# Kernel optimization log

Measured on AMD Instinct MI355X. Metric: run time of the kernel, lower is better.

Reference implementation:

```python
import jax, jax.numpy as jnp
import numpy as np

HIDDEN = 2048
NUM_HEADS = 16
HEAD_DIM = 128
WINDOW = 1024
ROPE_THETA = 10000.0
B, L = 1, 4096


def setup_inputs() -> dict:
    key = jax.random.key(0)
    k0, k1, k2, k3, k4 = jax.random.split(key, 5)
    s = 1.0 / np.sqrt(HIDDEN)
    return {
        "hidden_states": jax.random.normal(k0, (B, L, HIDDEN), dtype=jnp.float32),
        "wq": jax.random.normal(k1, (HIDDEN, NUM_HEADS * HEAD_DIM), dtype=jnp.float32) * s,
        "wk": jax.random.normal(k2, (HIDDEN, NUM_HEADS * HEAD_DIM), dtype=jnp.float32) * s,
        "wv": jax.random.normal(k3, (HIDDEN, NUM_HEADS * HEAD_DIM), dtype=jnp.float32) * s,
        "wo": jax.random.normal(k4, (NUM_HEADS * HEAD_DIM, HIDDEN), dtype=jnp.float32) * s,
    }


def _apply_rotary(x, cos, sin):
    # x: [B, H, L, D]; cos/sin: [L, D/2]
    d2 = x.shape[-1] // 2
    x1, x2 = x[..., :d2], x[..., d2:]
    return jnp.concatenate([x1 * cos - x2 * sin, x2 * cos + x1 * sin], axis=-1)


def reference(hidden_states, wq, wk, wv, wo):
    Bsz, Ln, _ = hidden_states.shape
    dtype = hidden_states.dtype
    scale = HEAD_DIM ** (-0.5)

    def split_heads(x):
        return x.reshape(Bsz, Ln, NUM_HEADS, HEAD_DIM).transpose(0, 2, 1, 3)

    q = split_heads(hidden_states @ wq)
    k = split_heads(hidden_states @ wk)
    v = split_heads(hidden_states @ wv)

    inv_freq = 1.0 / (ROPE_THETA ** (jnp.arange(0, HEAD_DIM, 2, dtype=jnp.float32) / HEAD_DIM))
    pos = jnp.arange(Ln, dtype=jnp.float32)
    freqs = pos[:, None] * inv_freq[None, :]  # [L, D/2]
    cos = jnp.cos(freqs).astype(dtype)
    sin = jnp.sin(freqs).astype(dtype)

    q = _apply_rotary(q, cos, sin)
    k = _apply_rotary(k, cos, sin)

    q_pos = jnp.arange(Ln)[:, None]
    k_pos = jnp.arange(Ln)[None, :]
    valid = (k_pos > q_pos - WINDOW) & (k_pos <= q_pos)  # [L, L]
    neg = jnp.finfo(dtype).min

    attn = jnp.einsum("bhqd,bhkd->bhqk", q, k) * scale
    attn = jnp.where(valid, attn, neg)
    attn = jax.nn.softmax(attn, axis=-1)
    out = jnp.einsum("bhqk,bhkd->bhqd", attn, v)
    out = out.transpose(0, 2, 1, 3).reshape(Bsz, Ln, NUM_HEADS * HEAD_DIM)
    return out @ wo
```

## Files before the change

kernel.cpp:

```cpp
#include <hip/hip_runtime.h>
#include <cstdint>
#include <cstddef>

typedef unsigned short u16;
typedef __bf16 bf16x8 __attribute__((ext_vector_type(8)));
typedef float f32x4 __attribute__((ext_vector_type(4)));
typedef unsigned short u16x8 __attribute__((ext_vector_type(8)));

#define SEQ 4096
#define HID 2048
#define NH 16
#define HD 128
#define WIN 1024

__device__ __forceinline__ float bf2f(u16 u) {
  union { unsigned int i; float f; } v; v.i = ((unsigned int)u) << 16; return v.f;
}
__device__ __forceinline__ u16 f2bf(float f) {
  union { float f; unsigned int i; } v; v.f = f;
  unsigned int r = v.i + 0x7FFFu + ((v.i >> 16) & 1u);
  return (u16)(r >> 16);
}
__device__ __forceinline__ u16 f2bf_rne(float f) {
  union { __bf16 b; u16 u; } v; v.b = (__bf16)f; return v.u;
}
__device__ __forceinline__ float exp2a(float x) {
  float r; asm("v_exp_f32 %0, %1" : "=v"(r) : "v"(x)); return r;
}
template<int L2R>
__device__ __forceinline__ unsigned swz(unsigned o) { return o ^ (((o >> L2R) & 7u) << 4); }

__device__ __forceinline__ void gload_lds16(const u16* g, u16* l) {
  __builtin_amdgcn_global_load_lds((const __attribute__((address_space(1))) void*)g,
                                   (__attribute__((address_space(3))) void*)l, 16, 0, 0);
}


__global__ void cast_f32_bf16(const float* __restrict__ in, u16* __restrict__ out, int n4) {
  int i = blockIdx.x * blockDim.x + threadIdx.x;
  if (i < n4) {
    float4 v = ((const float4*)in)[i];
    union { u16 u[4]; unsigned long long ll; } r;
    r.u[0] = f2bf(v.x); r.u[1] = f2bf(v.y); r.u[2] = f2bf(v.z); r.u[3] = f2bf(v.w);
    ((unsigned long long*)out)[i] = r.ll;
  }
}

__global__ void transpose_cast4(const float* __restrict__ w0, const float* __restrict__ w1,
                                const float* __restrict__ w2, const float* __restrict__ w3,
                                u16* __restrict__ o0, u16* __restrict__ o1,
                                u16* __restrict__ o2, u16* __restrict__ o3) {
  __shared__ float t[32][33];
  const float* W = (blockIdx.z == 0) ? w0 : (blockIdx.z == 1) ? w1 : (blockIdx.z == 2) ? w2 : w3;
  u16* Wt = (blockIdx.z == 0) ? o0 : (blockIdx.z == 1) ? o1 : (blockIdx.z == 2) ? o2 : o3;
  const int tx = threadIdx.x & 31, ty = threadIdx.x >> 5;
  const int x0 = blockIdx.x * 32, y0 = blockIdx.y * 32;
#pragma unroll
  for (int i = 0; i < 4; ++i)
    t[ty + i * 8][tx] = W[(size_t)(y0 + ty + i * 8) * HID + x0 + tx];
  __syncthreads();
#pragma unroll
  for (int i = 0; i < 4; ++i)
    Wt[(size_t)(x0 + ty + i * 8) * HID + y0 + tx] = f2bf(t[tx][ty + i * 8]);
}

__global__ void rope_table(float* __restrict__ ctab, float* __restrict__ stab) {
  int idx = blockIdx.x * blockDim.x + threadIdx.x;
  int pos = idx >> 6, i = idx & 63;
  float invf = expf(-(float)i * 0.14391156831212787f);
  float ang = (float)pos * invf;
  float s, c;
  sincosf(ang, &s, &c);
  ctab[idx] = c; stab[idx] = s;
}


__global__ __launch_bounds__(256, 2) void gemm_qkv_kernel(
    const u16* __restrict__ X, const u16* __restrict__ Wqt, const u16* __restrict__ Wkt,
    const u16* __restrict__ Wvt, u16* __restrict__ Qo, u16* __restrict__ Ko, u16* __restrict__ Vo,
    const float* __restrict__ ctab, const float* __restrict__ stab) {
  __shared__ u16 ldsA[2][8192];
  __shared__ u16 ldsB[2][8192];
  int flat = (blockIdx.z * 32 + blockIdx.y) * 16 + blockIdx.x;
  int nf = (flat & 7) * 192 + (flat >> 3);
  int bx = nf & 15, by = (nf >> 4) & 31, bz = nf >> 9;
  const u16* Bt = (bz == 0) ? Wqt : (bz == 1) ? Wkt : Wvt;
  u16* Cp = (bz == 0) ? Qo : (bz == 1) ? Ko : Vo;
  const int brow = by * 128, bcol = bx * 128;

  const int lane = threadIdx.x & 63;
  const int wv = threadIdx.x >> 6;
  const int g = lane >> 4, c = lane & 15;
  const int K = HID, N = HID;

  const f32x4 zero = {0.f, 0.f, 0.f, 0.f};
  f32x4 acc[2][8];
#pragma unroll
  for (int m = 0; m < 2; ++m)
#pragma unroll
    for (int n = 0; n < 8; ++n) acc[m][n] = zero;

  auto stage = [&](int buf, int kt) {
    const int k0 = kt * 64;
#pragma unroll
    for (int i = 0; i < 4; ++i) {
      unsigned o = ((unsigned)(wv * 4 + i) * 64 + (unsigned)lane) * 16u;
      unsigned r = o >> 7;
      unsigned cb = swz<7>(o) & 127u;
      const size_t gcol = (size_t)k0 + (cb >> 1);
      gload_lds16(X + (size_t)(brow + r) * K + gcol, &ldsA[buf][(wv * 4 + i) * 512]);
      gload_lds16(Bt + (size_t)(bcol + r) * K + gcol, &ldsB[buf][(wv * 4 + i) * 512]);
    }
  };

  stage(0, 0);
  __syncthreads();
  int buf = 0;
  const int nt = K / 64;
  for (int kt = 0; kt < nt; ++kt) {
    if (kt + 1 < nt) stage(buf ^ 1, kt + 1);
    __builtin_amdgcn_s_setprio(1);
#pragma unroll
    for (int s = 0; s < 2; ++s) {
      const unsigned kb = (unsigned)(s * 64 + g * 16);
      bf16x8 af[2], bfv[8];
#pragma unroll
      for (int m = 0; m < 2; ++m) {
        unsigned row = wv * 32 + m * 16 + c;
        af[m] = *(const bf16x8*)((const char*)&ldsA[buf][0] + swz<7>(row * 128 + kb));
      }
#pragma unroll
      for (int n = 0; n < 8; ++n) {
        unsigned row = n * 16 + c;
        bfv[n] = *(const bf16x8*)((const char*)&ldsB[buf][0] + swz<7>(row * 128 + kb));
      }
#pragma unroll
      for (int m = 0; m < 2; ++m)
#pragma unroll
        for (int n = 0; n < 8; ++n)
          acc[m][n] = __builtin_amdgcn_mfma_f32_16x16x32_bf16(af[m], bfv[n], acc[m][n], 0, 0, 0);
    }
    __builtin_amdgcn_s_setprio(0);
    __syncthreads();
    buf ^= 1;
  }

  if (bz < 2) {
#pragma unroll
    for (int m = 0; m < 2; ++m) {
      const int rbase = brow + wv * 32 + m * 16 + g * 4;
#pragma unroll
      for (int r = 0; r < 4; ++r) {
        const int pos = rbase + r;
        const float* cp = ctab + (size_t)pos * 64;
        const float* sp = stab + (size_t)pos * 64;
        u16* crow = Cp + (size_t)pos * N + bcol;
#pragma unroll
        for (int n = 0; n < 4; ++n) {
          const int i = n * 16 + c;
          const float x1 = acc[m][n][r], x2 = acc[m][n + 4][r];
          const float co = cp[i], si = sp[i];
          crow[i] = f2bf(x1 * co - x2 * si);
          crow[i + 64] = f2bf(x2 * co + x1 * si);
        }
      }
    }
  } else {
#pragma unroll
    for (int m = 0; m < 2; ++m) {
      const int rbase = brow + wv * 32 + m * 16 + g * 4;
#pragma unroll
      for (int r = 0; r < 4; ++r) {
        u16* crow = Cp + (size_t)(rbase + r) * N + bcol;
#pragma unroll
        for (int n = 0; n < 8; ++n)
          crow[n * 16 + c] = f2bf(acc[m][n][r]);
      }
    }
  }
}


__global__ __launch_bounds__(256, 2) void gemm_out_kernel(
    const u16* __restrict__ Ob, const u16* __restrict__ Wot, float* __restrict__ out) {
  __shared__ u16 ldsA[2][8192];
  __shared__ u16 ldsB[2][8192];
  int flat = blockIdx.y * 16 + blockIdx.x;
  int nf = (flat & 7) * 64 + (flat >> 3);
  int bx = nf & 15, by = nf >> 4;
  const int brow = by * 128, bcol = bx * 128;

  const int lane = threadIdx.x & 63;
  const int wv = threadIdx.x >> 6;
  const int wr = wv >> 1, wc = wv & 1;
  const int g = lane >> 4, c = lane & 15;
  const int K = HID, N = HID;

  const f32x4 zero = {0.f, 0.f, 0.f, 0.f};
  f32x4 acc[4][4];
#pragma unroll
  for (int m = 0; m < 4; ++m)
#pragma unroll
    for (int n = 0; n < 4; ++n) acc[m][n] = zero;

  auto stage = [&](int buf, int kt) {
    const int k0 = kt * 64;
#pragma unroll
    for (int i = 0; i < 4; ++i) {
      unsigned o = ((unsigned)(wv * 4 + i) * 64 + (unsigned)lane) * 16u;
      unsigned r = o >> 7;
      unsigned cb = swz<7>(o) & 127u;
      const size_t gcol = (size_t)k0 + (cb >> 1);
      gload_lds16(Ob + (size_t)(brow + r) * K + gcol, &ldsA[buf][(wv * 4 + i) * 512]);
      gload_lds16(Wot + (size_t)(bcol + r) * K + gcol, &ldsB[buf][(wv * 4 + i) * 512]);
    }
  };

  stage(0, 0);
  __syncthreads();
  int buf = 0;
  const int nt = K / 64;
  for (int kt = 0; kt < nt; ++kt) {
    if (kt + 1 < nt) stage(buf ^ 1, kt + 1);
    __builtin_amdgcn_s_setprio(1);
#pragma unroll
    for (int s = 0; s < 2; ++s) {
      const unsigned kb = (unsigned)(s * 64 + g * 16);
      bf16x8 af[4], bfv[4];
#pragma unroll
      for (int m = 0; m < 4; ++m) {
        unsigned row = wr * 64 + m * 16 + c;
        af[m] = *(const bf16x8*)((const char*)&ldsA[buf][0] + swz<7>(row * 128 + kb));
      }
#pragma unroll
      for (int n = 0; n < 4; ++n) {
        unsigned row = wc * 64 + n * 16 + c;
        bfv[n] = *(const bf16x8*)((const char*)&ldsB[buf][0] + swz<7>(row * 128 + kb));
      }
#pragma unroll
      for (int m = 0; m < 4; ++m)
#pragma unroll
        for (int n = 0; n < 4; ++n)
          acc[m][n] = __builtin_amdgcn_mfma_f32_16x16x32_bf16(af[m], bfv[n], acc[m][n], 0, 0, 0);
    }
    __builtin_amdgcn_s_setprio(0);
    __syncthreads();
    buf ^= 1;
  }

#pragma unroll
  for (int m = 0; m < 4; ++m) {
    const int rbase = brow + wr * 64 + m * 16 + g * 4;
#pragma unroll
    for (int n = 0; n < 4; ++n) {
      const int cbase = bcol + wc * 64 + n * 16 + c;
#pragma unroll
      for (int r = 0; r < 4; ++r)
        out[(size_t)(rbase + r) * N + cbase] = acc[m][n][r];
    }
  }
}


__global__ __launch_bounds__(256, 2) void attn_kernel(
    const u16* __restrict__ Q, const u16* __restrict__ K,
    const u16* __restrict__ V, u16* __restrict__ O) {
  __shared__ u16 k_lds[2][8192];
  __shared__ u16 vt_lds[2][8192];
  __shared__ u16 p_lds[4][1024];

  const int lane = threadIdx.x & 63;
  const int wv = threadIdx.x >> 6;
  const int g = lane >> 4;
  const int c = lane & 15;

  int flat = blockIdx.y * 64 + blockIdx.x;
  int nf = (flat & 7) * 128 + (flat >> 3);
  const int q0 = (nf & 63) * 64;
  const int h = nf >> 6;

#pragma unroll
  for (int i = 0; i < 4; ++i) {
    unsigned o = ((unsigned)(wv * 4 + i) * 64 + (unsigned)lane) * 16u;
    unsigned r = o >> 8;
    unsigned cb = swz<8>(o) & 255u;
    gload_lds16(Q + (size_t)(q0 + r) * HID + h * HD + (cb >> 1), &k_lds[0][(wv * 4 + i) * 512]);
  }
  __syncthreads();
  bf16x8 qf[4];
#pragma unroll
  for (int s = 0; s < 4; ++s) {
    unsigned row = wv * 16 + c;
    qf[s] = *(const bf16x8*)((const char*)&k_lds[0][0] + swz<8>(row * 256 + s * 64 + g * 16));
  }
  __syncthreads();

  const int t_start = (q0 >= WIN) ? (q0 - WIN) : 0;

#pragma unroll
  for (int i = 0; i < 4; ++i) {
    unsigned o = ((unsigned)(wv * 4 + i) * 64 + (unsigned)lane) * 16u;
    unsigned r = o >> 8;
    unsigned cb = swz<8>(o) & 255u;
    gload_lds16(K + (size_t)(t_start + r) * HID + h * HD + (cb >> 1), &k_lds[0][(wv * 4 + i) * 512]);
  }
  {
    const u16x8* src = (const u16x8*)(V + (size_t)(t_start + lane) * HID + h * HD + wv * 32);
#pragma unroll
    for (int it = 0; it < 4; ++it) {
      u16x8 vv = src[it];
#pragma unroll
      for (int j = 0; j < 8; ++j) {
        const int d = wv * 32 + it * 8 + j;
        vt_lds[0][d * 64 + (lane ^ ((d & 7) << 3))] = vv[j];
      }
    }
  }
  __syncthreads();

  const f32x4 zero = {0.f, 0.f, 0.f, 0.f};
  float mrow[4], lrow[4];
  f32x4 oacc[8];
#pragma unroll
  for (int r = 0; r < 4; ++r) { mrow[r] = -1e30f; lrow[r] = 0.f; }
#pragma unroll
  for (int d = 0; d < 8; ++d) oacc[d] = zero;

  const float scale2 = 0.12751743f;
  int b = 0;

  for (int t0 = t_start; t0 <= q0; t0 += 64) {
    const int nb = b ^ 1;
    const bool has_next = (t0 + 64 <= q0);

    u16x8 vr[4];
    if (has_next) {
#pragma unroll
      for (int i = 0; i < 4; ++i) {
        unsigned o = ((unsigned)(wv * 4 + i) * 64 + (unsigned)lane) * 16u;
        unsigned r = o >> 8;
        unsigned cb = swz<8>(o) & 255u;
        gload_lds16(K + (size_t)(t0 + 64 + r) * HID + h * HD + (cb >> 1),
                    &k_lds[nb][(wv * 4 + i) * 512]);
      }
      const u16x8* src = (const u16x8*)(V + (size_t)(t0 + 64 + lane) * HID + h * HD + wv * 32);
#pragma unroll
      for (int it = 0; it < 4; ++it) vr[it] = src[it];
    }

    f32x4 sa[4];
#pragma unroll
    for (int kf = 0; kf < 4; ++kf) sa[kf] = zero;
    __builtin_amdgcn_s_setprio(1);
#pragma unroll
    for (int s = 0; s < 4; ++s) {
#pragma unroll
      for (int kf = 0; kf < 4; ++kf) {
        unsigned row = kf * 16 + c;
        bf16x8 kb = *(const bf16x8*)((const char*)&k_lds[b][0] + swz<8>(row * 256 + s * 64 + g * 16));
        sa[kf] = __builtin_amdgcn_mfma_f32_16x16x32_bf16(qf[s], kb, sa[kf], 0, 0, 0);
      }
    }
    __builtin_amdgcn_s_setprio(0);

    const int qbase = q0 + wv * 16 + g * 4;
    const bool diag = (t0 == q0);
    const bool lowm = (q0 >= WIN) && (t0 == t_start);
    if (diag) {
#pragma unroll
      for (int kf = 0; kf < 4; ++kf) {
        const int kpos = t0 + kf * 16 + c;
#pragma unroll
        for (int r = 0; r < 4; ++r) {
          float x = sa[kf][r] * scale2;
          sa[kf][r] = (kpos <= qbase + r) ? x : -1e30f;
        }
      }
    } else if (lowm) {
#pragma unroll
      for (int kf = 0; kf < 4; ++kf) {
        const int kpos = t0 + kf * 16 + c;
#pragma unroll
        for (int r = 0; r < 4; ++r) {
          float x = sa[kf][r] * scale2;
          sa[kf][r] = (kpos > qbase + r - WIN) ? x : -1e30f;
        }
      }
    } else {
#pragma unroll
      for (int kf = 0; kf < 4; ++kf)
#pragma unroll
        for (int r = 0; r < 4; ++r) sa[kf][r] *= scale2;
    }

    float tmax[4];
#pragma unroll
    for (int r = 0; r < 4; ++r)
      tmax[r] = fmaxf(fmaxf(sa[0][r], sa[1][r]), fmaxf(sa[2][r], sa[3][r]));
#pragma unroll
    for (int r = 0; r < 4; ++r)
#pragma unroll
      for (int d = 1; d < 16; d <<= 1)
        tmax[r] = fmaxf(tmax[r], __shfl_xor(tmax[r], d, 16));

    bool okl = (tmax[0] <= mrow[0] + 8.f) && (tmax[1] <= mrow[1] + 8.f) &&
               (tmax[2] <= mrow[2] + 8.f) && (tmax[3] <= mrow[3] + 8.f);
    if (!__all((int)okl)) {
#pragma unroll
      for (int r = 0; r < 4; ++r) {
        const float mn = fmaxf(mrow[r], tmax[r]);
        const float al = exp2a(mrow[r] - mn);
        mrow[r] = mn;
        lrow[r] *= al;
#pragma unroll
        for (int df = 0; df < 8; ++df) oacc[df][r] *= al;
      }
    }

    float rs[4] = {0.f, 0.f, 0.f, 0.f};
    if (diag || lowm) {
#pragma unroll
      for (int kf = 0; kf < 4; ++kf)
#pragma unroll
        for (int r = 0; r < 4; ++r) {
          const float x = sa[kf][r];
          const float p = (x < -1e29f) ? 0.f : exp2a(x - mrow[r]);
          sa[kf][r] = p; rs[r] += p;
        }
    } else {
#pragma unroll
      for (int kf = 0; kf < 4; ++kf)
#pragma unroll
        for (int r = 0; r < 4; ++r) {
          const float p = exp2a(sa[kf][r] - mrow[r]);
          sa[kf][r] = p; rs[r] += p;
        }
    }
#pragma unroll
    for (int r = 0; r < 4; ++r) {
#pragma unroll
      for (int d = 1; d < 16; d <<= 1) rs[r] += __shfl_xor(rs[r], d, 16);
      lrow[r] += rs[r];
    }

#pragma unroll
    for (int kf = 0; kf < 4; ++kf)
#pragma unroll
      for (int r = 0; r < 4; ++r) {
        const int q = g * 4 + r;
        p_lds[wv][q * 64 + ((kf * 16 + c) ^ ((q & 7) << 3))] = f2bf_rne(sa[kf][r]);
      }

    if (has_next) {
#pragma unroll
      for (int it = 0; it < 4; ++it)
#pragma unroll
        for (int j = 0; j < 8; ++j) {
          const int d = wv * 32 + it * 8 + j;
          vt_lds[nb][d * 64 + (lane ^ ((d & 7) << 3))] = vr[it][j];
        }
    }

    asm volatile("" ::: "memory");

    __builtin_amdgcn_s_setprio(1);
#pragma unroll
    for (int s2 = 0; s2 < 2; ++s2) {
      const bf16x8 pa = *(const bf16x8*)&p_lds[wv][c * 64 + ((s2 * 32 + g * 8) ^ ((c & 7) << 3))];
#pragma unroll
      for (int df = 0; df < 8; ++df) {
        const int row = df * 16 + c;
        const bf16x8 vb = *(const bf16x8*)&vt_lds[b][row * 64 + ((s2 * 32 + g * 8) ^ ((row & 7) << 3))];
        oacc[df] = __builtin_amdgcn_mfma_f32_16x16x32_bf16(pa, vb, oacc[df], 0, 0, 0);
      }
    }
    __builtin_amdgcn_s_setprio(0);
    __syncthreads();
    b = nb;
  }

  float invl[4];
#pragma unroll
  for (int r = 0; r < 4; ++r) invl[r] = 1.f / lrow[r];
#pragma unroll
  for (int df = 0; df < 8; ++df)
#pragma unroll
    for (int r = 0; r < 4; ++r) {
      const int row = q0 + wv * 16 + g * 4 + r;
      const int col = h * HD + df * 16 + c;
      O[(size_t)row * HID + col] = f2bf(oacc[df][r] * invl[r]);
    }
}


extern "C" void kernel_launch(void* const* d_in, const int* in_sizes, int n_in,
                              void* d_out, int out_size, void* d_ws, size_t ws_size,
                              hipStream_t stream) {
  const float* hidden = (const float*)d_in[0];
  const float* wq = (const float*)d_in[1];
  const float* wk = (const float*)d_in[2];
  const float* wv = (const float*)d_in[3];
  const float* wo = (const float*)d_in[4];
  float* out = (float*)d_out;

  char* ws = (char*)d_ws;
  u16* Xb  = (u16*)ws;                 ws += (size_t)SEQ * HID * 2;
  u16* Wqt = (u16*)ws;                 ws += (size_t)HID * HID * 2;
  u16* Wkt = (u16*)ws;                 ws += (size_t)HID * HID * 2;
  u16* Wvt = (u16*)ws;                 ws += (size_t)HID * HID * 2;
  u16* Wot = (u16*)ws;                 ws += (size_t)HID * HID * 2;
  u16* Qb  = (u16*)ws;                 ws += (size_t)SEQ * HID * 2;
  u16* Kb  = (u16*)ws;                 ws += (size_t)SEQ * HID * 2;
  u16* Vb  = (u16*)ws;                 ws += (size_t)SEQ * HID * 2;
  u16* Ob  = (u16*)ws;                 ws += (size_t)SEQ * HID * 2;
  float* ctab = (float*)ws;            ws += (size_t)SEQ * 64 * 4;
  float* stab = (float*)ws;            ws += (size_t)SEQ * 64 * 4;

  cast_f32_bf16<<<(SEQ * HID / 4 + 255) / 256, 256, 0, stream>>>(hidden, Xb, SEQ * HID / 4);

  dim3 tg(64, 64, 4);
  transpose_cast4<<<tg, 256, 0, stream>>>(wq, wk, wv, wo, Wqt, Wkt, Wvt, Wot);

  rope_table<<<(SEQ * 64) / 256, 256, 0, stream>>>(ctab, stab);

  dim3 gq(HID / 128, SEQ / 128, 3);
  gemm_qkv_kernel<<<gq, 256, 0, stream>>>(Xb, Wqt, Wkt, Wvt, Qb, Kb, Vb, ctab, stab);

  dim3 ga(SEQ / 64, NH);
  attn_kernel<<<ga, 256, 0, stream>>>(Qb, Kb, Vb, Ob);

  dim3 go(HID / 128, SEQ / 128);
  gemm_out_kernel<<<go, 256, 0, stream>>>(Ob, Wot, out);
}
```

Before: 283.0 us.

## Compute transposed S in attention to keep P in registers, drop P LDS

The QK^T MFMA operands are swapped so each lane holds scores for a single query row, with key rows permuted during K staging. P can then be packed straight into bf16 MFMA A-operands in registers instead of round-tripping through LDS. Row max and sum reductions shrink to two cross-group shuffles. The V transpose buffer becomes single-buffered behind explicit barriers, and occupancy is raised to 3 blocks per CU. The cost is an extra barrier per iteration, V written to LDS after compute rather than overlapped, and shuffles to redistribute the rescale factors.

```diff
diff --git a/kernel.cpp b/kernel.cpp
--- a/kernel.cpp
+++ b/kernel.cpp
@@ -23,6 +23,9 @@
 }
 __device__ __forceinline__ u16 f2bf_rne(float f) {
   union { __bf16 b; u16 u; } v; v.b = (__bf16)f; return v.u;
+}
+__device__ __forceinline__ unsigned pk2(float lo, float hi) {
+  return (unsigned)f2bf_rne(lo) | ((unsigned)f2bf_rne(hi) << 16);
 }
 __device__ __forceinline__ float exp2a(float x) {
   float r; asm("v_exp_f32 %0, %1" : "=v"(r) : "v"(x)); return r;
@@ -262,12 +265,11 @@
 }
 
 
-__global__ __launch_bounds__(256, 2) void attn_kernel(
+__global__ __launch_bounds__(256, 3) void attn_kernel(
     const u16* __restrict__ Q, const u16* __restrict__ K,
     const u16* __restrict__ V, u16* __restrict__ O) {
   __shared__ u16 k_lds[2][8192];
-  __shared__ u16 vt_lds[2][8192];
-  __shared__ u16 p_lds[4][1024];
+  __shared__ u16 vt_lds[8192];
 
   const int lane = threadIdx.x & 63;
   const int wv = threadIdx.x >> 6;
@@ -278,6 +280,8 @@
   int nf = (flat & 7) * 128 + (flat >> 3);
   const int q0 = (nf & 63) * 64;
   const int h = nf >> 6;
+  const int qw = q0 + wv * 16;
+  const int qpos = qw + c;
 
 #pragma unroll
   for (int i = 0; i < 4; ++i) {
@@ -295,34 +299,44 @@
   }
   __syncthreads();
 
-  const int t_start = (q0 >= WIN) ? (q0 - WIN) : 0;
-
-#pragma unroll
-  for (int i = 0; i < 4; ++i) {
-    unsigned o = ((unsigned)(wv * 4 + i) * 64 + (unsigned)lane) * 16u;
-    unsigned r = o >> 8;
-    unsigned cb = swz<8>(o) & 255u;
-    gload_lds16(K + (size_t)(t_start + r) * HID + h * HD + (cb >> 1), &k_lds[0][(wv * 4 + i) * 512]);
-  }
-  {
-    const u16x8* src = (const u16x8*)(V + (size_t)(t_start + lane) * HID + h * HD + wv * 32);
-#pragma unroll
-    for (int it = 0; it < 4; ++it) {
-      u16x8 vv = src[it];
+  auto stageK = [&](int buf, int t0) {
+#pragma unroll
+    for (int i = 0; i < 4; ++i) {
+      unsigned o = ((unsigned)(wv * 4 + i) * 64 + (unsigned)lane) * 16u;
+      unsigned r = o >> 8;
+      unsigned key = (r & 0x23u) | ((r & 0x0Cu) << 1) | ((r & 0x10u) >> 2);
+      unsigned cb = swz<8>(o) & 255u;
+      gload_lds16(K + (size_t)(t0 + (int)key) * HID + h * HD + (cb >> 1),
+                  &k_lds[buf][(wv * 4 + i) * 512]);
+    }
+  };
+  u16x8 vr[4];
+  auto loadV = [&](int t0) {
+    const u16x8* src = (const u16x8*)(V + (size_t)(t0 + lane) * HID + h * HD + wv * 32);
+#pragma unroll
+    for (int it = 0; it < 4; ++it) vr[it] = src[it];
+  };
+  auto writeVT = [&]() {
+#pragma unroll
+    for (int it = 0; it < 4; ++it)
 #pragma unroll
       for (int j = 0; j < 8; ++j) {
         const int d = wv * 32 + it * 8 + j;
-        vt_lds[0][d * 64 + (lane ^ ((d & 7) << 3))] = vv[j];
-      }
-    }
-  }
+        vt_lds[d * 64 + (lane ^ ((d & 7) << 3))] = vr[it][j];
+      }
+  };
+
+  const int t_start = (q0 >= WIN) ? (q0 - WIN) : 0;
+
+  loadV(t_start);
+  stageK(0, t_start);
+  __syncthreads();
+  writeVT();
   __syncthreads();
 
   const f32x4 zero = {0.f, 0.f, 0.f, 0.f};
-  float mrow[4], lrow[4];
+  float mrow = -1e30f, lrow = 0.f;
   f32x4 oacc[8];
-#pragma unroll
-  for (int r = 0; r < 4; ++r) { mrow[r] = -1e30f; lrow[r] = 0.f; }
 #pragma unroll
   for (int d = 0; d < 8; ++d) oacc[d] = zero;
 
@@ -330,22 +344,10 @@
   int b = 0;
 
   for (int t0 = t_start; t0 <= q0; t0 += 64) {
-    const int nb = b ^ 1;
     const bool has_next = (t0 + 64 <= q0);
-
-    u16x8 vr[4];
     if (has_next) {
-#pragma unroll
-      for (int i = 0; i < 4; ++i) {
-        unsigned o = ((unsigned)(wv * 4 + i) * 64 + (unsigned)lane) * 16u;
-        unsigned r = o >> 8;
-        unsigned cb = swz<8>(o) & 255u;
-        gload_lds16(K + (size_t)(t0 + 64 + r) * HID + h * HD + (cb >> 1),
-                    &k_lds[nb][(wv * 4 + i) * 512]);
-      }
-      const u16x8* src = (const u16x8*)(V + (size_t)(t0 + 64 + lane) * HID + h * HD + wv * 32);
-#pragma unroll
-      for (int it = 0; it < 4; ++it) vr[it] = src[it];
+      loadV(t0 + 64);
+      stageK(b ^ 1, t0 + 64);
     }
 
     f32x4 sa[4];
@@ -358,32 +360,31 @@
       for (int kf = 0; kf < 4; ++kf) {
         unsigned row = kf * 16 + c;
         bf16x8 kb = *(const bf16x8*)((const char*)&k_lds[b][0] + swz<8>(row * 256 + s * 64 + g * 16));
-        sa[kf] = __builtin_amdgcn_mfma_f32_16x16x32_bf16(qf[s], kb, sa[kf], 0, 0, 0);
+        sa[kf] = __builtin_amdgcn_mfma_f32_16x16x32_bf16(kb, qf[s], sa[kf], 0, 0, 0);
       }
     }
     __builtin_amdgcn_s_setprio(0);
 
-    const int qbase = q0 + wv * 16 + g * 4;
     const bool diag = (t0 == q0);
     const bool lowm = (q0 >= WIN) && (t0 == t_start);
     if (diag) {
 #pragma unroll
       for (int kf = 0; kf < 4; ++kf) {
-        const int kpos = t0 + kf * 16 + c;
+        const int kbase = t0 + (kf >> 1) * 32 + g * 8 + (kf & 1) * 4;
 #pragma unroll
         for (int r = 0; r < 4; ++r) {
           float x = sa[kf][r] * scale2;
-          sa[kf][r] = (kpos <= qbase + r) ? x : -1e30f;
+          sa[kf][r] = (kbase + r <= qpos) ? x : -1e30f;
         }
       }
     } else if (lowm) {
 #pragma unroll
       for (int kf = 0; kf < 4; ++kf) {
-        const int kpos = t0 + kf * 16 + c;
+        const int kbase = t0 + (kf >> 1) * 32 + g * 8 + (kf & 1) * 4;
 #pragma unroll
         for (int r = 0; r < 4; ++r) {
           float x = sa[kf][r] * scale2;
-          sa[kf][r] = (kpos > qbase + r - WIN) ? x : -1e30f;
+          sa[kf][r] = (kbase + r > qpos - WIN) ? x : -1e30f;
         }
       }
     } else {
@@ -393,102 +394,93 @@
         for (int r = 0; r < 4; ++r) sa[kf][r] *= scale2;
     }
 
-    float tmax[4];
-#pragma unroll
-    for (int r = 0; r < 4; ++r)
-      tmax[r] = fmaxf(fmaxf(sa[0][r], sa[1][r]), fmaxf(sa[2][r], sa[3][r]));
-#pragma unroll
-    for (int r = 0; r < 4; ++r)
-#pragma unroll
-      for (int d = 1; d < 16; d <<= 1)
-        tmax[r] = fmaxf(tmax[r], __shfl_xor(tmax[r], d, 16));
-
-    bool okl = (tmax[0] <= mrow[0] + 8.f) && (tmax[1] <= mrow[1] + 8.f) &&
-               (tmax[2] <= mrow[2] + 8.f) && (tmax[3] <= mrow[3] + 8.f);
-    if (!__all((int)okl)) {
-#pragma unroll
-      for (int r = 0; r < 4; ++r) {
-        const float mn = fmaxf(mrow[r], tmax[r]);
-        const float al = exp2a(mrow[r] - mn);
-        mrow[r] = mn;
-        lrow[r] *= al;
-#pragma unroll
-        for (int df = 0; df < 8; ++df) oacc[df][r] *= al;
-      }
-    }
-
-    float rs[4] = {0.f, 0.f, 0.f, 0.f};
+    float tmax = -3e38f;
+#pragma unroll
+    for (int kf = 0; kf < 4; ++kf)
+#pragma unroll
+      for (int r = 0; r < 4; ++r) tmax = fmaxf(tmax, sa[kf][r]);
+    tmax = fmaxf(tmax, __shfl_xor(tmax, 16));
+    tmax = fmaxf(tmax, __shfl_xor(tmax, 32));
+
+    if (!__all((int)(tmax <= mrow + 8.f))) {
+      const float mn = fmaxf(mrow, tmax);
+      const float al = exp2a(mrow - mn);
+      mrow = mn;
+      lrow *= al;
+      float alo[4];
+#pragma unroll
+      for (int r = 0; r < 4; ++r) alo[r] = __shfl(al, (lane & 48) | (g * 4 + r));
+#pragma unroll
+      for (int df = 0; df < 8; ++df)
+#pragma unroll
+        for (int r = 0; r < 4; ++r) oacc[df][r] *= alo[r];
+    }
+
+    float rs = 0.f;
     if (diag || lowm) {
 #pragma unroll
       for (int kf = 0; kf < 4; ++kf)
 #pragma unroll
         for (int r = 0; r < 4; ++r) {
           const float x = sa[kf][r];
-          const float p = (x < -1e29f) ? 0.f : exp2a(x - mrow[r]);
-          sa[kf][r] = p; rs[r] += p;
+          const float p = (x < -1e29f) ? 0.f : exp2a(x - mrow);
+          sa[kf][r] = p; rs += p;
         }
     } else {
 #pragma unroll
       for (int kf = 0; kf < 4; ++kf)
 #pragma unroll
         for (int r = 0; r < 4; ++r) {
-          const float p = exp2a(sa[kf][r] - mrow[r]);
-          sa[kf][r] = p; rs[r] += p;
+          const float p = exp2a(sa[kf][r] - mrow);
+          sa[kf][r] = p; rs += p;
         }
     }
-#pragma unroll
-    for (int r = 0; r < 4; ++r) {
-#pragma unroll
-      for (int d = 1; d < 16; d <<= 1) rs[r] += __shfl_xor(rs[r], d, 16);
-      lrow[r] += rs[r];
-    }
-
-#pragma unroll
-    for (int kf = 0; kf < 4; ++kf)
-#pragma unroll
-      for (int r = 0; r < 4; ++r) {
-        const int q = g * 4 + r;
-        p_lds[wv][q * 64 + ((kf * 16 + c) ^ ((q & 7) << 3))] = f2bf_rne(sa[kf][r]);
-      }
-
-    if (has_next) {
-#pragma unroll
-      for (int it = 0; it < 4; ++it)
-#pragma unroll
-        for (int j = 0; j < 8; ++j) {
-          const int d = wv * 32 + it * 8 + j;
-          vt_lds[nb][d * 64 + (lane ^ ((d & 7) << 3))] = vr[it][j];
-        }
-    }
-
-    asm volatile("" ::: "memory");
+    rs += __shfl_xor(rs, 16);
+    rs += __shfl_xor(rs, 32);
+    lrow += rs;
+
+    union { bf16x8 v; unsigned u[4]; } pa0, pa1;
+    pa0.u[0] = pk2(sa[0][0], sa[0][1]); pa0.u[1] = pk2(sa[0][2], sa[0][3]);
+    pa0.u[2] = pk2(sa[1][0], sa[1][1]); pa0.u[3] = pk2(sa[1][2], sa[1][3]);
+    pa1.u[0] = pk2(sa[2][0], sa[2][1]); pa1.u[1] = pk2(sa[2][2], sa[2][3]);
+    pa1.u[2] = pk2(sa[3][0], sa[3][1]); pa1.u[3] = pk2(sa[3][2], sa[3][3]);
 
     __builtin_amdgcn_s_setprio(1);
 #pragma unroll
     for (int s2 = 0; s2 < 2; ++s2) {
-      const bf16x8 pa = *(const bf16x8*)&p_lds[wv][c * 64 + ((s2 * 32 + g * 8) ^ ((c & 7) << 3))];
+      const bf16x8 pa = s2 ? pa1.v : pa0.v;
 #pragma unroll
       for (int df = 0; df < 8; ++df) {
         const int row = df * 16 + c;
-        const bf16x8 vb = *(const bf16x8*)&vt_lds[b][row * 64 + ((s2 * 32 + g * 8) ^ ((row & 7) << 3))];
+        const bf16x8 vb = *(const bf16x8*)&vt_lds[row * 64 + ((s2 * 32 + g * 8) ^ ((row & 7) << 3))];
         oacc[df] = __builtin_amdgcn_mfma_f32_16x16x32_bf16(pa, vb, oacc[df], 0, 0, 0);
       }
     }
     __builtin_amdgcn_s_setprio(0);
-    __syncthreads();
-    b = nb;
-  }
-
-  float invl[4];
-#pragma unroll
-  for (int r = 0; r < 4; ++r) invl[r] = 1.f / lrow[r];
+
+    asm volatile("s_waitcnt lgkmcnt(0)" ::: "memory");
+    __builtin_amdgcn_s_barrier();
+
+    if (has_next) {
+      asm volatile("s_waitcnt vmcnt(4)" ::: "memory");
+      writeVT();
+    }
+    asm volatile("s_waitcnt vmcnt(0) lgkmcnt(0)" ::: "memory");
+    __builtin_amdgcn_s_barrier();
+    b ^= 1;
+  }
+
+  float ilo[4];
+  const float invl = 1.f / lrow;
+#pragma unroll
+  for (int r = 0; r < 4; ++r) ilo[r] = __shfl(invl, (lane & 48) | (g * 4 + r));
 #pragma unroll
   for (int df = 0; df < 8; ++df)
 #pragma unroll
     for (int r = 0; r < 4; ++r) {
-      const int row = q0 + wv * 16 + g * 4 + r;
+      const int row = qw + g * 4 + r;
       const int col = h * HD + df * 16 + c;
-      O[(size_t)row * HID + col] = f2bf(oacc[df][r] * invl[r]);
+      O[(size_t)row * HID + col] = f2bf(oacc[df][r] * ilo[r]);
     }
 }
 
```

Result: faster. 265.2 us (median of 2 runs) (-6.3%).
